# Performance work log

Hardware: AMD Instinct MI355X
Metric: run time of the kernel (lower is better)

The kernel has to match this reference:

```python
import jax, jax.numpy as jnp
import numpy as np

EMBED_DIM = 1024
NUM_HEADS = 16
HEAD_DIM = EMBED_DIM // NUM_HEADS
SCALE = HEAD_DIM ** -0.5
BATCH, SEQ = 2, 2048


def setup_inputs() -> dict:
    key = jax.random.key(0)
    k1, k2, k3 = jax.random.split(key, 3)
    # Xavier-uniform-like init scales
    s_qkv = (6.0 / (3 * EMBED_DIM + EMBED_DIM)) ** 0.5
    s_out = (6.0 / (2 * EMBED_DIM)) ** 0.5
    return {
        "x": jax.random.normal(k1, (BATCH, SEQ, EMBED_DIM), dtype=jnp.float32),
        "w_qkv": jax.random.uniform(k2, (3 * EMBED_DIM, EMBED_DIM), jnp.float32, -s_qkv, s_qkv),
        "w_out": jax.random.uniform(k3, (EMBED_DIM, EMBED_DIM), jnp.float32, -s_out, s_out),
        "bias_qkv": jnp.zeros((3 * EMBED_DIM,), jnp.float32),
        "bias_out": jnp.zeros((EMBED_DIM,), jnp.float32),
    }


def reference(x, w_qkv, w_out, bias_qkv, bias_out):
    B, S, E = x.shape
    H, D = NUM_HEADS, HEAD_DIM
    # Fused QKV projection: [B,S,3E]
    qkv = jnp.einsum('bse,fe->bsf', x, w_qkv) + bias_qkv
    q, k, v = jnp.split(qkv, 3, axis=-1)
    # [B,H,S,D]
    q = q.reshape(B, S, H, D).transpose(0, 2, 1, 3)
    k = k.reshape(B, S, H, D).transpose(0, 2, 1, 3)
    v = v.reshape(B, S, H, D).transpose(0, 2, 1, 3)
    # Scaled dot-product attention (non-causal, no mask)
    scores = jnp.einsum('bhqd,bhkd->bhqk', q, k) * SCALE
    attn = jax.nn.softmax(scores, axis=-1)
    ctx = jnp.einsum('bhqk,bhkd->bhqd', attn, v)
    ctx = ctx.transpose(0, 2, 1, 3).reshape(B, S, E)
    # Output projection
    return jnp.einsum('bse,fe->bsf', ctx, w_out) + bias_out
```

## Files before the change

### kernel.cpp

```cpp
#include <hip/hip_runtime.h>
#include <stdint.h>

#define B_ 2
#define S_ 2048
#define E_ 1024
#define H_ 16
#define D_ 64
#define QSCALE_ 0.18033688011112042f

typedef __attribute__((ext_vector_type(8))) short short8;
typedef __attribute__((ext_vector_type(4))) float f32x4;
typedef __attribute__((ext_vector_type(16))) float f32x16;
typedef unsigned int u32;

__device__ __forceinline__ unsigned short f2bf(float x) {
    union { float f; u32 u; } v; v.f = x;
    u32 r = v.u + 0x7fffu + ((v.u >> 16) & 1u);
    return (unsigned short)(r >> 16);
}
__device__ __forceinline__ u32 fbits(float x) {
    union { float f; u32 u; } v; v.f = x; return v.u;
}
__device__ __forceinline__ u32 pkbf(float lo, float hi) {
    return __builtin_amdgcn_perm(fbits(hi), fbits(lo), 0x07060302u);
}

__device__ __forceinline__ f32x4 mfma16(short8 a, short8 b, f32x4 c) {
    return __builtin_amdgcn_mfma_f32_16x16x32_bf16(a, b, c, 0, 0, 0);
}
__device__ __forceinline__ f32x16 mfma32(short8 a, short8 b, f32x16 c) {
    return __builtin_amdgcn_mfma_f32_32x32x16_bf16(a, b, c, 0, 0, 0);
}

__device__ __forceinline__ void gld16(const unsigned short* g, unsigned short* l) {
    __builtin_amdgcn_global_load_lds(
        (const __attribute__((address_space(1))) u32*)g,
        (__attribute__((address_space(3))) u32*)l, 16, 0, 0);
}

__global__ __launch_bounds__(256) void cvt_kernel(
    const float* __restrict__ x, const float* __restrict__ wq,
    const float* __restrict__ wo,
    unsigned short* __restrict__ xb, unsigned short* __restrict__ wqb,
    unsigned short* __restrict__ wob)
{
    const long i8 = ((long)blockIdx.x * 256 + threadIdx.x) * 8;
    const float* src; unsigned short* dst; long off;
    if (i8 < 4194304)      { src = x;  dst = xb;  off = i8; }
    else if (i8 < 7340032) { src = wq; dst = wqb; off = i8 - 4194304; }
    else                   { src = wo; dst = wob; off = i8 - 7340032; }
    f32x4 a = *(const f32x4*)(src + off);
    f32x4 b = *(const f32x4*)(src + off + 4);
    short8 o;
    o[0] = (short)f2bf(a[0]); o[1] = (short)f2bf(a[1]);
    o[2] = (short)f2bf(a[2]); o[3] = (short)f2bf(a[3]);
    o[4] = (short)f2bf(b[0]); o[5] = (short)f2bf(b[1]);
    o[6] = (short)f2bf(b[2]); o[7] = (short)f2bf(b[3]);
    *(short8*)(dst + off) = o;
}

__global__ __launch_bounds__(256) void qkv_gemm_kernel(
    const unsigned short* __restrict__ x, const unsigned short* __restrict__ w,
    const float* __restrict__ bias,
    unsigned short* __restrict__ Qg, unsigned short* __restrict__ Kg,
    unsigned short* __restrict__ Vtg)
{
    __shared__ __attribute__((aligned(16))) unsigned char smem[16896];
    __shared__ float biass[128];
    unsigned short* As = (unsigned short*)smem;
    unsigned short* Bs = (unsigned short*)(smem + 8192);
    float* Tr = (float*)smem;

    const int t = threadIdx.x;
    const int m0 = blockIdx.x * 128;
    const int n0 = blockIdx.y * 128;
    const int lane = t & 63;
    const int wv = t >> 6;
    const int g = lane >> 4;
    const int l15 = lane & 15;
    const int wm = (wv >> 1) * 64;
    const int wn = (wv & 1) * 64;
    const int rloc = lane >> 2;
    const int cg = (lane & 3) ^ ((lane >> 3) & 3);
    const int rsw = (g ^ ((l15 >> 1) & 3)) * 8;

    if (t < 128) biass[t] = bias[n0 + t];

    f32x4 acc[4][4];
#pragma unroll
    for (int i = 0; i < 4; ++i)
#pragma unroll
        for (int j = 0; j < 4; ++j)
            acc[i][j] = (f32x4){0.f, 0.f, 0.f, 0.f};

    for (int kt = 0; kt < E_; kt += 32) {
        __syncthreads();
#pragma unroll
        for (int j = 0; j < 2; ++j) {
            const int rb = 32 * wv + 16 * j;
            gld16(x + (m0 + rb + rloc) * E_ + kt + cg * 8, &As[rb * 32]);
            gld16(w + (n0 + rb + rloc) * E_ + kt + cg * 8, &Bs[rb * 32]);
        }
        __syncthreads();

        short8 af[4], bf[4];
#pragma unroll
        for (int mt = 0; mt < 4; ++mt)
            af[mt] = *(const short8*)&As[(wm + mt * 16 + l15) * 32 + rsw];
#pragma unroll
        for (int nt = 0; nt < 4; ++nt)
            bf[nt] = *(const short8*)&Bs[(wn + nt * 16 + l15) * 32 + rsw];
#pragma unroll
        for (int mt = 0; mt < 4; ++mt)
#pragma unroll
            for (int nt = 0; nt < 4; ++nt)
                acc[mt][nt] = mfma16(af[mt], bf[nt], acc[mt][nt]);
    }

    if (n0 < 2048) {
#pragma unroll
        for (int mt = 0; mt < 4; ++mt) {
#pragma unroll
            for (int nt = 0; nt < 4; ++nt) {
                const int col = n0 + wn + nt * 16 + l15;
                const int which = col >> 10;
                const int cr = col & 1023;
                const int h = cr >> 6;
                const int d = cr & 63;
                const float bia = biass[col - n0];
#pragma unroll
                for (int i = 0; i < 4; ++i) {
                    const int row = m0 + wm + mt * 16 + g * 4 + i;
                    const int bb = row >> 11;
                    const int s = row & 2047;
                    const int bh = bb * H_ + h;
                    const float v = acc[mt][nt][i] + bia;
                    if (which == 0)
                        Qg[(bh * S_ + s) * D_ + d] = f2bf(v * QSCALE_);
                    else
                        Kg[(bh * S_ + s) * D_ + d] = f2bf(v);
                }
            }
        }
    } else {
        const int bb = m0 >> 11;
        const int s0 = m0 & 2047;
        const int dth = t >> 3;
        const int sc = t & 7;
#pragma unroll
        for (int sl = 0; sl < 4; ++sl) {
            __syncthreads();
            if ((wv & 1) == (sl >> 1)) {
#pragma unroll
                for (int q = 0; q < 2; ++q) {
                    const int nt = (sl & 1) * 2 + q;
                    const float bia = biass[wn + nt * 16 + l15];
                    const int dloc = q * 16 + l15;
#pragma unroll
                    for (int mt = 0; mt < 4; ++mt)
#pragma unroll
                        for (int i = 0; i < 4; ++i)
                            Tr[(wm + mt * 16 + g * 4 + i) * 33 + dloc] =
                                acc[mt][nt][i] + bia;
                }
            }
            __syncthreads();
            const int dglob = (n0 - 2048) + sl * 32 + dth;
            const int h = dglob >> 6;
            const int dd = dglob & 63;
            unsigned short* dst =
                Vtg + ((long)(bb * H_ + h) * D_ + dd) * S_ + s0 + sc * 16;
            short8 o0, o1;
#pragma unroll
            for (int j = 0; j < 4; ++j) {
                o0[j]     = (short)f2bf(Tr[(sc * 16 + j)      * 33 + dth]);
                o0[4 + j] = (short)f2bf(Tr[(sc * 16 + 8 + j)  * 33 + dth]);
                o1[j]     = (short)f2bf(Tr[(sc * 16 + 4 + j)  * 33 + dth]);
                o1[4 + j] = (short)f2bf(Tr[(sc * 16 + 12 + j) * 33 + dth]);
            }
            *(short8*)dst = o0;
            *(short8*)(dst + 8) = o1;
        }
    }
}

__global__ __launch_bounds__(64, 1) void attn_kernel(
    const unsigned short* __restrict__ Qg, const unsigned short* __restrict__ Kg,
    const unsigned short* __restrict__ Vtg, unsigned short* __restrict__ ctx)
{
    __shared__ __attribute__((aligned(16))) unsigned short Ks[2][64 * 64];
    __shared__ __attribute__((aligned(16))) unsigned short Vs[2][64 * 64];
    __shared__ float lsumbuf[64];

    const int lane = threadIdx.x;
    const int qb = blockIdx.x;
    const int bh = blockIdx.y;
    const int bb = bh >> 4;
    const int hh = bh & 15;
    const int l31 = lane & 31;
    const int hf = lane >> 5;
    const int rloc = lane >> 3;
    const int cg = (lane & 7) ^ ((lane >> 3) & 7);
    const int sw = l31 & 7;

    short8 qa[2][4];
#pragma unroll
    for (int qh = 0; qh < 2; ++qh)
#pragma unroll
        for (int kc = 0; kc < 4; ++kc)
            qa[qh][kc] = *(const short8*)(
                Qg + (bh * S_ + qb * 64 + qh * 32 + l31) * D_ + kc * 16 + hf * 8);

    f32x16 O[2][2];
    float lsum[2] = {0.f, 0.f};
#pragma unroll
    for (int qh = 0; qh < 2; ++qh)
#pragma unroll
        for (int dt = 0; dt < 2; ++dt)
#pragma unroll
            for (int r = 0; r < 16; ++r) O[qh][dt][r] = 0.f;

    auto stage = [&](int kb2, int bufi) {
#pragma unroll
        for (int i = 0; i < 8; ++i)
            gld16(Kg + (bh * S_ + kb2 * 64 + i * 8 + rloc) * D_ + cg * 8,
                  &Ks[bufi][i * 512]);
#pragma unroll
        for (int i = 0; i < 8; ++i)
            gld16(Vtg + (bh * D_ + i * 8 + rloc) * S_ + kb2 * 64 + cg * 8,
                  &Vs[bufi][i * 512]);
    };

    stage(0, 0);

    for (int kb = 0; kb < S_ / 64; ++kb) {
        __builtin_amdgcn_s_waitcnt(0);
        __syncthreads();
        if (kb + 1 < S_ / 64) stage(kb + 1, (kb + 1) & 1);
        const unsigned short* ks = Ks[kb & 1];
        const unsigned short* vs = Vs[kb & 1];

        f32x16 st[2][2];
#pragma unroll
        for (int kt = 0; kt < 2; ++kt) {
            short8 kf[4];
#pragma unroll
            for (int kc = 0; kc < 4; ++kc)
                kf[kc] = *(const short8*)&ks[(kt * 32 + l31) * 64 + ((2 * kc + hf) ^ sw) * 8];
#pragma unroll
            for (int qh = 0; qh < 2; ++qh) {
                f32x16 s;
#pragma unroll
                for (int r = 0; r < 16; ++r) s[r] = 0.f;
#pragma unroll
                for (int kc = 0; kc < 4; ++kc)
                    s = mfma32(kf[kc], qa[qh][kc], s);
                st[kt][qh] = s;
            }
        }

#pragma unroll
        for (int kt = 0; kt < 2; ++kt) {
#pragma unroll
            for (int cp = 0; cp < 2; ++cp) {
                short8 vb[2];
#pragma unroll
                for (int dt = 0; dt < 2; ++dt)
                    vb[dt] = *(const short8*)&vs[(dt * 32 + l31) * 64 +
                                                 ((4 * kt + 2 * cp + hf) ^ sw) * 8];
#pragma unroll
                for (int qh = 0; qh < 2; ++qh) {
                    float p[8];
#pragma unroll
                    for (int j = 0; j < 8; ++j)
                        p[j] = __builtin_amdgcn_exp2f(st[kt][qh][8 * cp + j]);
                    lsum[qh] += (p[0] + p[1]) + (p[2] + p[3]) +
                                (p[4] + p[5]) + (p[6] + p[7]);
                    union { short8 s8; u32 u[4]; } pa;
                    pa.u[0] = pkbf(p[0], p[1]);
                    pa.u[1] = pkbf(p[2], p[3]);
                    pa.u[2] = pkbf(p[4], p[5]);
                    pa.u[3] = pkbf(p[6], p[7]);
#pragma unroll
                    for (int dt = 0; dt < 2; ++dt)
                        O[qh][dt] = mfma32(pa.s8, vb[dt], O[qh][dt]);
                }
            }
        }
    }

#pragma unroll
    for (int qh = 0; qh < 2; ++qh) {
        float s = lsum[qh] + __shfl_xor(lsum[qh], 32);
        if (hf == 0) lsumbuf[qh * 32 + l31] = s;
    }
    __builtin_amdgcn_s_waitcnt(0);
    __syncthreads();
    float inv[2][16];
#pragma unroll
    for (int qh = 0; qh < 2; ++qh)
#pragma unroll
        for (int r = 0; r < 16; ++r) {
            const int ql = qh * 32 + 4 * hf + (r & 3) + 8 * (r >> 2);
            inv[qh][r] = 1.0f / lsumbuf[ql];
        }

#pragma unroll
    for (int qh = 0; qh < 2; ++qh)
#pragma unroll
        for (int dt = 0; dt < 2; ++dt)
#pragma unroll
            for (int r = 0; r < 16; ++r) {
                const int ql = qh * 32 + 4 * hf + (r & 3) + 8 * (r >> 2);
                const int s = qb * 64 + ql;
                ctx[(bb * S_ + s) * E_ + hh * D_ + dt * 32 + l31] =
                    f2bf(O[qh][dt][r] * inv[qh][r]);
            }
}

__global__ __launch_bounds__(256) void out_gemm_kernel(
    const unsigned short* __restrict__ ctxg, const unsigned short* __restrict__ w,
    const float* __restrict__ bias, float* __restrict__ out)
{
    __shared__ __attribute__((aligned(16))) unsigned short As[128 * 32];
    __shared__ __attribute__((aligned(16))) unsigned short Bs[64 * 32];
    __shared__ float biass[64];

    const int t = threadIdx.x;
    const int m0 = blockIdx.x * 128;
    const int n0 = blockIdx.y * 64;
    const int lane = t & 63;
    const int wv = t >> 6;
    const int g = lane >> 4;
    const int l15 = lane & 15;
    const int wm = (wv >> 1) * 64;
    const int wn = (wv & 1) * 32;
    const int rloc = lane >> 2;
    const int cg = (lane & 3) ^ ((lane >> 3) & 3);
    const int rsw = (g ^ ((l15 >> 1) & 3)) * 8;

    if (t < 64) biass[t] = bias[n0 + t];

    f32x4 acc[4][2];
#pragma unroll
    for (int i = 0; i < 4; ++i)
#pragma unroll
        for (int j = 0; j < 2; ++j)
            acc[i][j] = (f32x4){0.f, 0.f, 0.f, 0.f};

    for (int kt = 0; kt < E_; kt += 32) {
        __syncthreads();
#pragma unroll
        for (int j = 0; j < 2; ++j) {
            const int rb = 32 * wv + 16 * j;
            gld16(ctxg + (m0 + rb + rloc) * E_ + kt + cg * 8, &As[rb * 32]);
        }
        {
            const int rb = 16 * wv;
            gld16(w + (n0 + rb + rloc) * E_ + kt + cg * 8, &Bs[rb * 32]);
        }
        __syncthreads();

        short8 af[4], bf[2];
#pragma unroll
        for (int mt = 0; mt < 4; ++mt)
            af[mt] = *(const short8*)&As[(wm + mt * 16 + l15) * 32 + rsw];
#pragma unroll
        for (int nt = 0; nt < 2; ++nt)
            bf[nt] = *(const short8*)&Bs[(wn + nt * 16 + l15) * 32 + rsw];
#pragma unroll
        for (int mt = 0; mt < 4; ++mt)
#pragma unroll
            for (int nt = 0; nt < 2; ++nt)
                acc[mt][nt] = mfma16(af[mt], bf[nt], acc[mt][nt]);
    }

#pragma unroll
    for (int mt = 0; mt < 4; ++mt) {
#pragma unroll
        for (int nt = 0; nt < 2; ++nt) {
            const int col = n0 + wn + nt * 16 + l15;
            const float bia = biass[col - n0];
#pragma unroll
            for (int i = 0; i < 4; ++i) {
                const int row = m0 + wm + mt * 16 + g * 4 + i;
                out[row * E_ + col] = acc[mt][nt][i] + bia;
            }
        }
    }
}

extern "C" void kernel_launch(void* const* d_in, const int* in_sizes, int n_in,
                              void* d_out, int out_size, void* d_ws, size_t ws_size,
                              hipStream_t stream) {
    const float* x    = (const float*)d_in[0];
    const float* wqkv = (const float*)d_in[1];
    const float* wout = (const float*)d_in[2];
    const float* bqkv = (const float*)d_in[3];
    const float* bout = (const float*)d_in[4];

    unsigned short* Q   = (unsigned short*)d_ws;
    unsigned short* K   = Q + 4194304;
    unsigned short* Vt  = K + 4194304;
    unsigned short* ctx = Vt + 4194304;
    unsigned short* xb  = ctx;
    unsigned short* wqb = ctx + 4194304;
    unsigned short* wob = wqb + 3145728;

    cvt_kernel<<<4096, 256, 0, stream>>>(x, wqkv, wout, xb, wqb, wob);
    qkv_gemm_kernel<<<dim3(32, 24), 256, 0, stream>>>(xb, wqb, bqkv, Q, K, Vt);
    attn_kernel<<<dim3(32, 32), 64, 0, stream>>>(Q, K, Vt, ctx);
    out_gemm_kernel<<<dim3(32, 16), 256, 0, stream>>>(ctx, wob, bout, (float*)d_out);
}
```

Measured before the change: 191.2 us.

## Widen GEMM K-tiles to 64 and share K/V tiles across two attention waves

Both projection GEMMs now stage 64-wide K slices per iteration with an 8-way XOR swizzle, which halves the number of barrier-separated load/compute rounds. The attention kernel now runs two waves per block over 128 query rows. The two waves share one double-buffered K/V tile, with one wave loading K and the other loading V, which halves global K/V traffic per query row. The explicit waitcnt before the barrier and the barrier around the row-sum buffer are removed. This lowers sync cost but may race if the asynchronous LDS loads are not drained before the barrier.

```diff
diff --git a/kernel.cpp b/kernel.cpp
--- a/kernel.cpp
+++ b/kernel.cpp
@@ -65,10 +65,10 @@
     unsigned short* __restrict__ Qg, unsigned short* __restrict__ Kg,
     unsigned short* __restrict__ Vtg)
 {
-    __shared__ __attribute__((aligned(16))) unsigned char smem[16896];
+    __shared__ __attribute__((aligned(16))) unsigned char smem[32768];
     __shared__ float biass[128];
     unsigned short* As = (unsigned short*)smem;
-    unsigned short* Bs = (unsigned short*)(smem + 8192);
+    unsigned short* Bs = (unsigned short*)(smem + 16384);
     float* Tr = (float*)smem;
 
     const int t = threadIdx.x;
@@ -80,9 +80,8 @@
     const int l15 = lane & 15;
     const int wm = (wv >> 1) * 64;
     const int wn = (wv & 1) * 64;
-    const int rloc = lane >> 2;
-    const int cg = (lane & 3) ^ ((lane >> 3) & 3);
-    const int rsw = (g ^ ((l15 >> 1) & 3)) * 8;
+    const int rloc = lane >> 3;
+    const int cg = (lane & 7) ^ (rloc & 7);
 
     if (t < 128) biass[t] = bias[n0 + t];
 
@@ -93,28 +92,33 @@
         for (int j = 0; j < 4; ++j)
             acc[i][j] = (f32x4){0.f, 0.f, 0.f, 0.f};
 
-    for (int kt = 0; kt < E_; kt += 32) {
+    for (int kt = 0; kt < E_; kt += 64) {
         __syncthreads();
 #pragma unroll
-        for (int j = 0; j < 2; ++j) {
-            const int rb = 32 * wv + 16 * j;
-            gld16(x + (m0 + rb + rloc) * E_ + kt + cg * 8, &As[rb * 32]);
-            gld16(w + (n0 + rb + rloc) * E_ + kt + cg * 8, &Bs[rb * 32]);
+        for (int j = 0; j < 4; ++j) {
+            const int rb = 32 * wv + 8 * j;
+            gld16(x + (m0 + rb + rloc) * E_ + kt + cg * 8, &As[rb * 64]);
+            gld16(w + (n0 + rb + rloc) * E_ + kt + cg * 8, &Bs[rb * 64]);
         }
         __syncthreads();
 
-        short8 af[4], bf[4];
-#pragma unroll
-        for (int mt = 0; mt < 4; ++mt)
-            af[mt] = *(const short8*)&As[(wm + mt * 16 + l15) * 32 + rsw];
-#pragma unroll
-        for (int nt = 0; nt < 4; ++nt)
-            bf[nt] = *(const short8*)&Bs[(wn + nt * 16 + l15) * 32 + rsw];
-#pragma unroll
-        for (int mt = 0; mt < 4; ++mt)
+#pragma unroll
+        for (int ks = 0; ks < 2; ++ks) {
+            short8 af[4], bf[4];
+#pragma unroll
+            for (int mt = 0; mt < 4; ++mt)
+                af[mt] = *(const short8*)&As[(wm + mt * 16 + l15) * 64 +
+                                             (((ks * 4 + g) ^ (l15 & 7)) * 8)];
 #pragma unroll
             for (int nt = 0; nt < 4; ++nt)
-                acc[mt][nt] = mfma16(af[mt], bf[nt], acc[mt][nt]);
+                bf[nt] = *(const short8*)&Bs[(wn + nt * 16 + l15) * 64 +
+                                             (((ks * 4 + g) ^ (l15 & 7)) * 8)];
+#pragma unroll
+            for (int mt = 0; mt < 4; ++mt)
+#pragma unroll
+                for (int nt = 0; nt < 4; ++nt)
+                    acc[mt][nt] = mfma16(af[mt], bf[nt], acc[mt][nt]);
+        }
     }
 
     if (n0 < 2048) {
@@ -184,15 +188,17 @@
     }
 }
 
-__global__ __launch_bounds__(64, 1) void attn_kernel(
+__global__ __launch_bounds__(128) void attn_kernel(
     const unsigned short* __restrict__ Qg, const unsigned short* __restrict__ Kg,
     const unsigned short* __restrict__ Vtg, unsigned short* __restrict__ ctx)
 {
     __shared__ __attribute__((aligned(16))) unsigned short Ks[2][64 * 64];
     __shared__ __attribute__((aligned(16))) unsigned short Vs[2][64 * 64];
-    __shared__ float lsumbuf[64];
-
-    const int lane = threadIdx.x;
+    __shared__ float lsumbuf[128];
+
+    const int t = threadIdx.x;
+    const int lane = t & 63;
+    const int wv = t >> 6;
     const int qb = blockIdx.x;
     const int bh = blockIdx.y;
     const int bb = bh >> 4;
@@ -200,16 +206,17 @@
     const int l31 = lane & 31;
     const int hf = lane >> 5;
     const int rloc = lane >> 3;
-    const int cg = (lane & 7) ^ ((lane >> 3) & 7);
+    const int cg = (lane & 7) ^ (rloc & 7);
     const int sw = l31 & 7;
 
+    const int qrow0 = qb * 128 + wv * 64;
     short8 qa[2][4];
 #pragma unroll
     for (int qh = 0; qh < 2; ++qh)
 #pragma unroll
         for (int kc = 0; kc < 4; ++kc)
             qa[qh][kc] = *(const short8*)(
-                Qg + (bh * S_ + qb * 64 + qh * 32 + l31) * D_ + kc * 16 + hf * 8);
+                Qg + (bh * S_ + qrow0 + qh * 32 + l31) * D_ + kc * 16 + hf * 8);
 
     f32x16 O[2][2];
     float lsum[2] = {0.f, 0.f};
@@ -221,20 +228,22 @@
             for (int r = 0; r < 16; ++r) O[qh][dt][r] = 0.f;
 
     auto stage = [&](int kb2, int bufi) {
-#pragma unroll
-        for (int i = 0; i < 8; ++i)
-            gld16(Kg + (bh * S_ + kb2 * 64 + i * 8 + rloc) * D_ + cg * 8,
-                  &Ks[bufi][i * 512]);
-#pragma unroll
-        for (int i = 0; i < 8; ++i)
-            gld16(Vtg + (bh * D_ + i * 8 + rloc) * S_ + kb2 * 64 + cg * 8,
-                  &Vs[bufi][i * 512]);
+        if (wv == 0) {
+#pragma unroll
+            for (int i = 0; i < 8; ++i)
+                gld16(Kg + (bh * S_ + kb2 * 64 + i * 8 + rloc) * D_ + cg * 8,
+                      &Ks[bufi][i * 512]);
+        } else {
+#pragma unroll
+            for (int i = 0; i < 8; ++i)
+                gld16(Vtg + (bh * D_ + i * 8 + rloc) * S_ + kb2 * 64 + cg * 8,
+                      &Vs[bufi][i * 512]);
+        }
     };
 
     stage(0, 0);
 
     for (int kb = 0; kb < S_ / 64; ++kb) {
-        __builtin_amdgcn_s_waitcnt(0);
         __syncthreads();
         if (kb + 1 < S_ / 64) stage(kb + 1, (kb + 1) & 1);
         const unsigned short* ks = Ks[kb & 1];
@@ -292,17 +301,15 @@
 #pragma unroll
     for (int qh = 0; qh < 2; ++qh) {
         float s = lsum[qh] + __shfl_xor(lsum[qh], 32);
-        if (hf == 0) lsumbuf[qh * 32 + l31] = s;
-    }
-    __builtin_amdgcn_s_waitcnt(0);
-    __syncthreads();
+        if (hf == 0) lsumbuf[wv * 64 + qh * 32 + l31] = s;
+    }
     float inv[2][16];
 #pragma unroll
     for (int qh = 0; qh < 2; ++qh)
 #pragma unroll
         for (int r = 0; r < 16; ++r) {
             const int ql = qh * 32 + 4 * hf + (r & 3) + 8 * (r >> 2);
-            inv[qh][r] = 1.0f / lsumbuf[ql];
+            inv[qh][r] = 1.0f / lsumbuf[wv * 64 + ql];
         }
 
 #pragma unroll
@@ -312,7 +319,7 @@
 #pragma unroll
             for (int r = 0; r < 16; ++r) {
                 const int ql = qh * 32 + 4 * hf + (r & 3) + 8 * (r >> 2);
-                const int s = qb * 64 + ql;
+                const int s = qb * 128 + wv * 64 + ql;
                 ctx[(bb * S_ + s) * E_ + hh * D_ + dt * 32 + l31] =
                     f2bf(O[qh][dt][r] * inv[qh][r]);
             }
@@ -322,8 +329,8 @@
     const unsigned short* __restrict__ ctxg, const unsigned short* __restrict__ w,
     const float* __restrict__ bias, float* __restrict__ out)
 {
-    __shared__ __attribute__((aligned(16))) unsigned short As[128 * 32];
-    __shared__ __attribute__((aligned(16))) unsigned short Bs[64 * 32];
+    __shared__ __attribute__((aligned(16))) unsigned short As[128 * 64];
+    __shared__ __attribute__((aligned(16))) unsigned short Bs[64 * 64];
     __shared__ float biass[64];
 
     const int t = threadIdx.x;
@@ -335,9 +342,8 @@
     const int l15 = lane & 15;
     const int wm = (wv >> 1) * 64;
     const int wn = (wv & 1) * 32;
-    const int rloc = lane >> 2;
-    const int cg = (lane & 3) ^ ((lane >> 3) & 3);
-    const int rsw = (g ^ ((l15 >> 1) & 3)) * 8;
+    const int rloc = lane >> 3;
+    const int cg = (lane & 7) ^ (rloc & 7);
 
     if (t < 64) biass[t] = bias[n0 + t];
 
@@ -348,31 +354,37 @@
         for (int j = 0; j < 2; ++j)
             acc[i][j] = (f32x4){0.f, 0.f, 0.f, 0.f};
 
-    for (int kt = 0; kt < E_; kt += 32) {
+    for (int kt = 0; kt < E_; kt += 64) {
         __syncthreads();
 #pragma unroll
+        for (int j = 0; j < 4; ++j) {
+            const int rb = 32 * wv + 8 * j;
+            gld16(ctxg + (m0 + rb + rloc) * E_ + kt + cg * 8, &As[rb * 64]);
+        }
+#pragma unroll
         for (int j = 0; j < 2; ++j) {
-            const int rb = 32 * wv + 16 * j;
-            gld16(ctxg + (m0 + rb + rloc) * E_ + kt + cg * 8, &As[rb * 32]);
-        }
-        {
-            const int rb = 16 * wv;
-            gld16(w + (n0 + rb + rloc) * E_ + kt + cg * 8, &Bs[rb * 32]);
+            const int rb = 16 * wv + 8 * j;
+            gld16(w + (n0 + rb + rloc) * E_ + kt + cg * 8, &Bs[rb * 64]);
         }
         __syncthreads();
 
-        short8 af[4], bf[2];
-#pragma unroll
-        for (int mt = 0; mt < 4; ++mt)
-            af[mt] = *(const short8*)&As[(wm + mt * 16 + l15) * 32 + rsw];
-#pragma unroll
-        for (int nt = 0; nt < 2; ++nt)
-            bf[nt] = *(const short8*)&Bs[(wn + nt * 16 + l15) * 32 + rsw];
-#pragma unroll
-        for (int mt = 0; mt < 4; ++mt)
+#pragma unroll
+        for (int ks = 0; ks < 2; ++ks) {
+            short8 af[4], bf[2];
+#pragma unroll
+            for (int mt = 0; mt < 4; ++mt)
+                af[mt] = *(const short8*)&As[(wm + mt * 16 + l15) * 64 +
+                                             (((ks * 4 + g) ^ (l15 & 7)) * 8)];
 #pragma unroll
             for (int nt = 0; nt < 2; ++nt)
-                acc[mt][nt] = mfma16(af[mt], bf[nt], acc[mt][nt]);
+                bf[nt] = *(const short8*)&Bs[(wn + nt * 16 + l15) * 64 +
+                                             (((ks * 4 + g) ^ (l15 & 7)) * 8)];
+#pragma unroll
+            for (int mt = 0; mt < 4; ++mt)
+#pragma unroll
+                for (int nt = 0; nt < 2; ++nt)
+                    acc[mt][nt] = mfma16(af[mt], bf[nt], acc[mt][nt]);
+        }
     }
 
 #pragma unroll
@@ -409,6 +421,6 @@
 
     cvt_kernel<<<4096, 256, 0, stream>>>(x, wqkv, wout, xb, wqb, wob);
     qkv_gemm_kernel<<<dim3(32, 24), 256, 0, stream>>>(xb, wqb, bqkv, Q, K, Vt);
-    attn_kernel<<<dim3(32, 32), 64, 0, stream>>>(Q, K, Vt, ctx);
+    attn_kernel<<<dim3(16, 32), 128, 0, stream>>>(Q, K, Vt, ctx);
     out_gemm_kernel<<<dim3(32, 16), 256, 0, stream>>>(ctx, wob, bout, (float*)d_out);
 }
```

After: 200.1 us. +4.6%, slower.

## Split attention key range across four waves and reduce partial outputs in LDS

Applied to the files above, without the earlier changes.

The attention kernel goes from one wave per 64-query block to four waves. Each wave handles a quarter of the key sequence and reads K and V fragments straight from global memory, so the LDS double-buffered staging is gone. The per-wave partial outputs and row sums are combined with shared-memory float atomics, then normalized and written out as bf16 with vector stores. This raises parallelism per block and shortens the serial key loop, at the cost of uncoalesced global K/V reads and an LDS atomic reduction. The softmax still needs no running max because the scores are unnormalized exp2 with a global scale.

```diff
diff --git a/kernel.cpp b/kernel.cpp
--- a/kernel.cpp
+++ b/kernel.cpp
@@ -184,24 +184,30 @@
     }
 }
 
-__global__ __launch_bounds__(64, 1) void attn_kernel(
+__global__ __launch_bounds__(256, 3) void attn_kernel(
     const unsigned short* __restrict__ Qg, const unsigned short* __restrict__ Kg,
     const unsigned short* __restrict__ Vtg, unsigned short* __restrict__ ctx)
 {
-    __shared__ __attribute__((aligned(16))) unsigned short Ks[2][64 * 64];
-    __shared__ __attribute__((aligned(16))) unsigned short Vs[2][64 * 64];
-    __shared__ float lsumbuf[64];
-
-    const int lane = threadIdx.x;
+    __shared__ float Oacc[64 * 64];
+    __shared__ float lsumW[4][64];
+
+    const int t = threadIdx.x;
+    const int lane = t & 63;
+    const int wv = t >> 6;
     const int qb = blockIdx.x;
     const int bh = blockIdx.y;
     const int bb = bh >> 4;
     const int hh = bh & 15;
     const int l31 = lane & 31;
     const int hf = lane >> 5;
-    const int rloc = lane >> 3;
-    const int cg = (lane & 7) ^ ((lane >> 3) & 7);
-    const int sw = l31 & 7;
+
+    {
+        f32x4 z = (f32x4){0.f, 0.f, 0.f, 0.f};
+#pragma unroll
+        for (int i = 0; i < 4; ++i)
+            *(f32x4*)&Oacc[t * 16 + i * 4] = z;
+    }
+    __syncthreads();
 
     short8 qa[2][4];
 #pragma unroll
@@ -220,33 +226,21 @@
 #pragma unroll
             for (int r = 0; r < 16; ++r) O[qh][dt][r] = 0.f;
 
-    auto stage = [&](int kb2, int bufi) {
-#pragma unroll
-        for (int i = 0; i < 8; ++i)
-            gld16(Kg + (bh * S_ + kb2 * 64 + i * 8 + rloc) * D_ + cg * 8,
-                  &Ks[bufi][i * 512]);
-#pragma unroll
-        for (int i = 0; i < 8; ++i)
-            gld16(Vtg + (bh * D_ + i * 8 + rloc) * S_ + kb2 * 64 + cg * 8,
-                  &Vs[bufi][i * 512]);
-    };
-
-    stage(0, 0);
-
-    for (int kb = 0; kb < S_ / 64; ++kb) {
-        __builtin_amdgcn_s_waitcnt(0);
-        __syncthreads();
-        if (kb + 1 < S_ / 64) stage(kb + 1, (kb + 1) & 1);
-        const unsigned short* ks = Ks[kb & 1];
-        const unsigned short* vs = Vs[kb & 1];
-
-        f32x16 st[2][2];
+    const unsigned short* Kbase = Kg + (bh * S_ + l31) * D_ + hf * 8;
+    const unsigned short* Vb0 = Vtg + (bh * D_ + l31) * S_;
+    const unsigned short* Vb1 = Vtg + (bh * D_ + 32 + l31) * S_;
+
+    for (int i = 0; i < 8; ++i) {
+        const int kb = wv * 8 + i;
+        const int ko = kb * 64;
 #pragma unroll
         for (int kt = 0; kt < 2; ++kt) {
             short8 kf[4];
 #pragma unroll
             for (int kc = 0; kc < 4; ++kc)
-                kf[kc] = *(const short8*)&ks[(kt * 32 + l31) * 64 + ((2 * kc + hf) ^ sw) * 8];
+                kf[kc] = *(const short8*)(Kbase + (ko + kt * 32) * D_ + kc * 16);
+
+            f32x16 st[2];
 #pragma unroll
             for (int qh = 0; qh < 2; ++qh) {
                 f32x16 s;
@@ -255,25 +249,20 @@
 #pragma unroll
                 for (int kc = 0; kc < 4; ++kc)
                     s = mfma32(kf[kc], qa[qh][kc], s);
-                st[kt][qh] = s;
-            }
-        }
-
-#pragma unroll
-        for (int kt = 0; kt < 2; ++kt) {
+                st[qh] = s;
+            }
+
 #pragma unroll
             for (int cp = 0; cp < 2; ++cp) {
-                short8 vb[2];
-#pragma unroll
-                for (int dt = 0; dt < 2; ++dt)
-                    vb[dt] = *(const short8*)&vs[(dt * 32 + l31) * 64 +
-                                                 ((4 * kt + 2 * cp + hf) ^ sw) * 8];
+                const int vo = ko + kt * 32 + cp * 16 + hf * 8;
+                short8 vb0 = *(const short8*)(Vb0 + vo);
+                short8 vb1 = *(const short8*)(Vb1 + vo);
 #pragma unroll
                 for (int qh = 0; qh < 2; ++qh) {
                     float p[8];
 #pragma unroll
                     for (int j = 0; j < 8; ++j)
-                        p[j] = __builtin_amdgcn_exp2f(st[kt][qh][8 * cp + j]);
+                        p[j] = __builtin_amdgcn_exp2f(st[qh][8 * cp + j]);
                     lsum[qh] += (p[0] + p[1]) + (p[2] + p[3]) +
                                 (p[4] + p[5]) + (p[6] + p[7]);
                     union { short8 s8; u32 u[4]; } pa;
@@ -281,9 +270,8 @@
                     pa.u[1] = pkbf(p[2], p[3]);
                     pa.u[2] = pkbf(p[4], p[5]);
                     pa.u[3] = pkbf(p[6], p[7]);
-#pragma unroll
-                    for (int dt = 0; dt < 2; ++dt)
-                        O[qh][dt] = mfma32(pa.s8, vb[dt], O[qh][dt]);
+                    O[qh][0] = mfma32(pa.s8, vb0, O[qh][0]);
+                    O[qh][1] = mfma32(pa.s8, vb1, O[qh][1]);
                 }
             }
         }
@@ -292,30 +280,36 @@
 #pragma unroll
     for (int qh = 0; qh < 2; ++qh) {
         float s = lsum[qh] + __shfl_xor(lsum[qh], 32);
-        if (hf == 0) lsumbuf[qh * 32 + l31] = s;
-    }
-    __builtin_amdgcn_s_waitcnt(0);
+        if (hf == 0) lsumW[wv][qh * 32 + l31] = s;
+    }
+#pragma unroll
+    for (int qh = 0; qh < 2; ++qh)
+#pragma unroll
+        for (int dt = 0; dt < 2; ++dt)
+#pragma unroll
+            for (int r = 0; r < 16; ++r) {
+                const int q = qh * 32 + 4 * hf + (r & 3) + 8 * (r >> 2);
+                atomicAdd(&Oacc[q * 64 + dt * 32 + l31], O[qh][dt][r]);
+            }
     __syncthreads();
-    float inv[2][16];
-#pragma unroll
-    for (int qh = 0; qh < 2; ++qh)
-#pragma unroll
-        for (int r = 0; r < 16; ++r) {
-            const int ql = qh * 32 + 4 * hf + (r & 3) + 8 * (r >> 2);
-            inv[qh][r] = 1.0f / lsumbuf[ql];
-        }
-
-#pragma unroll
-    for (int qh = 0; qh < 2; ++qh)
-#pragma unroll
-        for (int dt = 0; dt < 2; ++dt)
-#pragma unroll
-            for (int r = 0; r < 16; ++r) {
-                const int ql = qh * 32 + 4 * hf + (r & 3) + 8 * (r >> 2);
-                const int s = qb * 64 + ql;
-                ctx[(bb * S_ + s) * E_ + hh * D_ + dt * 32 + l31] =
-                    f2bf(O[qh][dt][r] * inv[qh][r]);
-            }
+
+    {
+        const int q = t >> 2;
+        const int c = t & 3;
+        const float inv = 1.0f / (lsumW[0][q] + lsumW[1][q] +
+                                  lsumW[2][q] + lsumW[3][q]);
+        const float* src = &Oacc[q * 64 + c * 16];
+        unsigned short* dst =
+            ctx + ((long)(bb * S_ + qb * 64 + q)) * E_ + hh * D_ + c * 16;
+        short8 o0, o1;
+#pragma unroll
+        for (int j = 0; j < 8; ++j) {
+            o0[j] = (short)f2bf(src[j] * inv);
+            o1[j] = (short)f2bf(src[8 + j] * inv);
+        }
+        *(short8*)dst = o0;
+        *(short8*)(dst + 8) = o1;
+    }
 }
 
 __global__ __launch_bounds__(256) void out_gemm_kernel(
@@ -409,6 +403,6 @@
 
     cvt_kernel<<<4096, 256, 0, stream>>>(x, wqkv, wout, xb, wqb, wob);
     qkv_gemm_kernel<<<dim3(32, 24), 256, 0, stream>>>(xb, wqb, bqkv, Q, K, Vt);
-    attn_kernel<<<dim3(32, 32), 64, 0, stream>>>(Q, K, Vt, ctx);
+    attn_kernel<<<dim3(32, 32), 256, 0, stream>>>(Q, K, Vt, ctx);
     out_gemm_kernel<<<dim3(32, 16), 256, 0, stream>>>(ctx, wob, bout, (float*)d_out);
 }
```

Result: slower. 333.5 us (+74.4%).

## Share K/V tiles across waves and split KV range within attention block

Applied to the files above, without the earlier changes.

The attention kernel goes from one 64-thread wave per block to four waves per block. Two waves cover two 64-row query sub-tiles and share the same K/V LDS tiles, with one wave loading K and the other loading V. Two such pairs each process half of the KV sequence. Their unnormalised outputs and row sums are combined through an LDS overlay before normalisation. This is meant to cut global K/V traffic per query row and raise latency hiding, at the cost of extra barriers, an LDS reduction and reliance on __syncthreads to cover the async loads now that the explicit waitcnt is gone.

```diff
diff --git a/kernel.cpp b/kernel.cpp
--- a/kernel.cpp
+++ b/kernel.cpp
@@ -184,15 +184,23 @@
     }
 }
 
-__global__ __launch_bounds__(64, 1) void attn_kernel(
+__global__ __launch_bounds__(256, 2) void attn_kernel(
     const unsigned short* __restrict__ Qg, const unsigned short* __restrict__ Kg,
     const unsigned short* __restrict__ Vtg, unsigned short* __restrict__ ctx)
 {
-    __shared__ __attribute__((aligned(16))) unsigned short Ks[2][64 * 64];
-    __shared__ __attribute__((aligned(16))) unsigned short Vs[2][64 * 64];
-    __shared__ float lsumbuf[64];
-
-    const int lane = threadIdx.x;
+    __shared__ __attribute__((aligned(16))) unsigned char smem[65536];
+    __shared__ float lsumbuf[4][64];
+    unsigned short* KsA = (unsigned short*)smem;
+    unsigned short* VsA = (unsigned short*)(smem + 16384);
+    unsigned short* KsB = (unsigned short*)(smem + 32768);
+    unsigned short* VsB = (unsigned short*)(smem + 49152);
+    float* overlay = (float*)smem;
+
+    const int t = threadIdx.x;
+    const int lane = t & 63;
+    const int wv = t >> 6;
+    const int pair = wv >> 1;
+    const int qsub = wv & 1;
     const int qb = blockIdx.x;
     const int bh = blockIdx.y;
     const int bb = bh >> 4;
@@ -200,16 +208,20 @@
     const int l31 = lane & 31;
     const int hf = lane >> 5;
     const int rloc = lane >> 3;
-    const int cg = (lane & 7) ^ ((lane >> 3) & 7);
+    const int cg = (lane & 7) ^ (rloc & 7);
     const int sw = l31 & 7;
 
+    unsigned short* Ks = pair ? KsB : KsA;
+    unsigned short* Vs = pair ? VsB : VsA;
+
+    const int qrow0 = qb * 128 + qsub * 64;
     short8 qa[2][4];
 #pragma unroll
     for (int qh = 0; qh < 2; ++qh)
 #pragma unroll
         for (int kc = 0; kc < 4; ++kc)
             qa[qh][kc] = *(const short8*)(
-                Qg + (bh * S_ + qb * 64 + qh * 32 + l31) * D_ + kc * 16 + hf * 8);
+                Qg + (bh * S_ + qrow0 + qh * 32 + l31) * D_ + kc * 16 + hf * 8);
 
     f32x16 O[2][2];
     float lsum[2] = {0.f, 0.f};
@@ -220,25 +232,28 @@
 #pragma unroll
             for (int r = 0; r < 16; ++r) O[qh][dt][r] = 0.f;
 
-    auto stage = [&](int kb2, int bufi) {
-#pragma unroll
-        for (int i = 0; i < 8; ++i)
-            gld16(Kg + (bh * S_ + kb2 * 64 + i * 8 + rloc) * D_ + cg * 8,
-                  &Ks[bufi][i * 512]);
-#pragma unroll
-        for (int i = 0; i < 8; ++i)
-            gld16(Vtg + (bh * D_ + i * 8 + rloc) * S_ + kb2 * 64 + cg * 8,
-                  &Vs[bufi][i * 512]);
+    auto stage = [&](int it, int bufi) {
+        const int tile = pair * 16 + it;
+        if ((wv & 1) == 0) {
+#pragma unroll
+            for (int i = 0; i < 8; ++i)
+                gld16(Kg + (bh * S_ + tile * 64 + i * 8 + rloc) * D_ + cg * 8,
+                      Ks + bufi * 4096 + i * 512);
+        } else {
+#pragma unroll
+            for (int i = 0; i < 8; ++i)
+                gld16(Vtg + (bh * D_ + i * 8 + rloc) * S_ + tile * 64 + cg * 8,
+                      Vs + bufi * 4096 + i * 512);
+        }
     };
 
     stage(0, 0);
 
-    for (int kb = 0; kb < S_ / 64; ++kb) {
-        __builtin_amdgcn_s_waitcnt(0);
+    for (int it = 0; it < 16; ++it) {
         __syncthreads();
-        if (kb + 1 < S_ / 64) stage(kb + 1, (kb + 1) & 1);
-        const unsigned short* ks = Ks[kb & 1];
-        const unsigned short* vs = Vs[kb & 1];
+        if (it + 1 < 16) stage(it + 1, (it + 1) & 1);
+        const unsigned short* ks = Ks + (it & 1) * 4096;
+        const unsigned short* vs = Vs + (it & 1) * 4096;
 
         f32x16 st[2][2];
 #pragma unroll
@@ -292,30 +307,45 @@
 #pragma unroll
     for (int qh = 0; qh < 2; ++qh) {
         float s = lsum[qh] + __shfl_xor(lsum[qh], 32);
-        if (hf == 0) lsumbuf[qh * 32 + l31] = s;
-    }
-    __builtin_amdgcn_s_waitcnt(0);
+        if (hf == 0) lsumbuf[wv][qh * 32 + l31] = s;
+    }
     __syncthreads();
-    float inv[2][16];
-#pragma unroll
-    for (int qh = 0; qh < 2; ++qh)
-#pragma unroll
-        for (int r = 0; r < 16; ++r) {
-            const int ql = qh * 32 + 4 * hf + (r & 3) + 8 * (r >> 2);
-            inv[qh][r] = 1.0f / lsumbuf[ql];
-        }
-
-#pragma unroll
-    for (int qh = 0; qh < 2; ++qh)
-#pragma unroll
-        for (int dt = 0; dt < 2; ++dt)
+
+    if (pair == 1) {
+#pragma unroll
+        for (int qh = 0; qh < 2; ++qh)
+#pragma unroll
+            for (int dt = 0; dt < 2; ++dt)
+#pragma unroll
+                for (int r = 0; r < 16; ++r) {
+                    const int ql = qh * 32 + 4 * hf + (r & 3) + 8 * (r >> 2);
+                    overlay[qsub * 4096 + ql * 64 + dt * 32 + l31] = O[qh][dt][r];
+                }
+    }
+    __syncthreads();
+
+    if (pair == 0) {
+        float inv[2][16];
+#pragma unroll
+        for (int qh = 0; qh < 2; ++qh)
 #pragma unroll
             for (int r = 0; r < 16; ++r) {
                 const int ql = qh * 32 + 4 * hf + (r & 3) + 8 * (r >> 2);
-                const int s = qb * 64 + ql;
-                ctx[(bb * S_ + s) * E_ + hh * D_ + dt * 32 + l31] =
-                    f2bf(O[qh][dt][r] * inv[qh][r]);
-            }
+                inv[qh][r] = 1.0f / (lsumbuf[wv][ql] + lsumbuf[wv + 2][ql]);
+            }
+#pragma unroll
+        for (int qh = 0; qh < 2; ++qh)
+#pragma unroll
+            for (int dt = 0; dt < 2; ++dt)
+#pragma unroll
+                for (int r = 0; r < 16; ++r) {
+                    const int ql = qh * 32 + 4 * hf + (r & 3) + 8 * (r >> 2);
+                    const float v = (O[qh][dt][r] +
+                        overlay[qsub * 4096 + ql * 64 + dt * 32 + l31]) * inv[qh][r];
+                    const int s = qb * 128 + qsub * 64 + ql;
+                    ctx[(bb * S_ + s) * E_ + hh * D_ + dt * 32 + l31] = f2bf(v);
+                }
+    }
 }
 
 __global__ __launch_bounds__(256) void out_gemm_kernel(
@@ -409,6 +439,6 @@
 
     cvt_kernel<<<4096, 256, 0, stream>>>(x, wqkv, wout, xb, wqb, wob);
     qkv_gemm_kernel<<<dim3(32, 24), 256, 0, stream>>>(xb, wqb, bqkv, Q, K, Vt);
-    attn_kernel<<<dim3(32, 32), 64, 0, stream>>>(Q, K, Vt, ctx);
+    attn_kernel<<<dim3(16, 32), 256, 0, stream>>>(Q, K, Vt, ctx);
     out_gemm_kernel<<<dim3(32, 16), 256, 0, stream>>>(ctx, wob, bout, (float*)d_out);
 }
```

After: 180.7 us. 1.06x faster.
